# Kernel optimization log

Hardware: AMD Instinct MI355X
Metric: run time of the kernel (lower is better)

## Reference

```python
import jax, jax.numpy as jnp
import numpy as np

N = 100000
E = 1600000
D_IN = 64
D_HID = 64


def setup_inputs() -> dict:
    key = jax.random.key(0)
    k_x, k_e, k_w1, k_w2 = jax.random.split(key, 4)
    x = jax.random.normal(k_x, (N, D_IN), dtype=jnp.float32)
    edge_index = jax.random.randint(k_e, (2, E), 0, N, dtype=jnp.int64)
    # Glorot-ish init for GCNConv linear weights, bias zeros (PyG default bias=True)
    W1 = jax.random.normal(k_w1, (D_IN, D_HID), dtype=jnp.float32) * (1.0 / np.sqrt(D_IN))
    b1 = jnp.zeros((D_HID,), dtype=jnp.float32)
    W2 = jax.random.normal(k_w2, (D_HID, D_HID), dtype=jnp.float32) * (1.0 / np.sqrt(D_HID))
    b2 = jnp.zeros((D_HID,), dtype=jnp.float32)
    return {"x": x, "W1": W1, "b1": b1, "W2": W2, "b2": b2, "edge_index": edge_index}


def _gcn_norm(edge_index, n):
    # PyG GCNConv default: add self-loops, symmetric normalization D^-1/2 A D^-1/2
    loop = jnp.arange(n, dtype=edge_index.dtype)
    src = jnp.concatenate([edge_index[0], loop])  # [E+N] message sources (j)
    dst = jnp.concatenate([edge_index[1], loop])  # [E+N] message targets (i)
    ones = jnp.ones_like(dst, dtype=jnp.float32)
    deg = jax.ops.segment_sum(ones, dst, num_segments=n)  # in-degree incl. self-loop
    deg_inv_sqrt = jnp.where(deg > 0, jax.lax.rsqrt(deg), 0.0)
    norm = deg_inv_sqrt[src] * deg_inv_sqrt[dst]  # [E+N]
    return src, dst, norm


def _gcn_conv(x, W, b, src, dst, norm, n):
    h = x @ W                                   # [N, D_out] dense transform first
    msg = h[src] * norm[:, None]                # gather + edge scale, [E+N, D_out]
    out = jax.ops.segment_sum(msg, dst, num_segments=n)  # scatter-add to targets
    return out + b


def reference(x, W1, b1, W2, b2, edge_index):
    n = x.shape[0]
    src, dst, norm = _gcn_norm(edge_index, n)
    h = _gcn_conv(x, W1, b1, src, dst, norm, n)
    h = jax.nn.relu(h)
    out = _gcn_conv(h, W2, b2, src, dst, norm, n)
    return out
```

## Files before the change

### kernel.cpp

```cpp
#include <hip/hip_runtime.h>
#include <hip/hip_bf16.h>

constexpr int D = 64;
constexpr int CAP = 64;
constexpr int NBUCK = 8;

__global__ void k_fill_pad(const int* __restrict__ src, const int* __restrict__ dst,
                           int* __restrict__ cur, int* __restrict__ csr,
                           int e, int bdiv) {
    int p = blockIdx.x & (NBUCK - 1);
    int sub = blockIdx.x >> 3;
    int nsub = gridDim.x >> 3;
    int lo = p * bdiv, hi = lo + bdiv;
    for (int i = sub * blockDim.x + threadIdx.x; i < e; i += nsub * blockDim.x) {
        int d = dst[i];
        if (d >= lo && d < hi) {
            int r = atomicAdd(&cur[d], 1);
            if (r < CAP) csr[((size_t)d << 6) + r] = src[i];
        }
    }
}

__global__ void k_prep(const float* __restrict__ x, __hip_bfloat16* __restrict__ xb,
                       const int* __restrict__ cur, float* __restrict__ dinv, int n) {
    int stride = gridDim.x * blockDim.x;
    int i0 = blockIdx.x * blockDim.x + threadIdx.x;
    for (int i = i0; i < n; i += stride)
        dinv[i] = rsqrtf((float)cur[i] + 1.0f);
    int total = n * D;
    for (int i = i0; i < total; i += stride)
        xb[i] = __float2bfloat16(x[i]);
}

template <bool STORE_RELU_BF16>
__launch_bounds__(256, 2)
__global__ void k_agg_mm(const __hip_bfloat16* __restrict__ xin, const float* __restrict__ W,
                         const float* __restrict__ b, const int* __restrict__ csr,
                         const int* __restrict__ cnt, const float* __restrict__ dinv,
                         float* __restrict__ outf, __hip_bfloat16* __restrict__ outb, int n) {
    int lane = threadIdx.x & 63;
    float w[D];
#pragma unroll
    for (int k = 0; k < D; ++k) w[k] = W[k * D + lane];
    float bias = b[lane];

    int wv = __builtin_amdgcn_readfirstlane(threadIdx.x >> 6);
    int wave = blockIdx.x * (blockDim.x >> 6) + wv;
    int nwaves = gridDim.x * (blockDim.x >> 6);

    for (int node = wave; node < n; node += nwaves) {
        float dnode = dinv[node];
        float acc = __bfloat162float(xin[((size_t)node << 6) + lane]) * dnode;
        const int* __restrict__ row = csr + ((size_t)node << 6);
        int deg = cnt[node];
        deg = deg > CAP ? CAP : deg;
        int j = 0;
        for (; j + 7 < deg; j += 8) {
            int s0 = row[j], s1 = row[j + 1], s2 = row[j + 2], s3 = row[j + 3];
            int s4 = row[j + 4], s5 = row[j + 5], s6 = row[j + 6], s7 = row[j + 7];
            float v0 = __bfloat162float(xin[((size_t)s0 << 6) + lane]);
            float v1 = __bfloat162float(xin[((size_t)s1 << 6) + lane]);
            float v2 = __bfloat162float(xin[((size_t)s2 << 6) + lane]);
            float v3 = __bfloat162float(xin[((size_t)s3 << 6) + lane]);
            float v4 = __bfloat162float(xin[((size_t)s4 << 6) + lane]);
            float v5 = __bfloat162float(xin[((size_t)s5 << 6) + lane]);
            float v6 = __bfloat162float(xin[((size_t)s6 << 6) + lane]);
            float v7 = __bfloat162float(xin[((size_t)s7 << 6) + lane]);
            acc = fmaf(v0, dinv[s0], acc);
            acc = fmaf(v1, dinv[s1], acc);
            acc = fmaf(v2, dinv[s2], acc);
            acc = fmaf(v3, dinv[s3], acc);
            acc = fmaf(v4, dinv[s4], acc);
            acc = fmaf(v5, dinv[s5], acc);
            acc = fmaf(v6, dinv[s6], acc);
            acc = fmaf(v7, dinv[s7], acc);
        }
        for (; j < deg; ++j) {
            int s = row[j];
            acc = fmaf(__bfloat162float(xin[((size_t)s << 6) + lane]), dinv[s], acc);
        }
        acc *= dnode;

        int ab = __float_as_int(acc);
        float o0 = bias, o1 = 0.f;
#pragma unroll
        for (int k = 0; k < D; k += 2) {
            float a0 = __int_as_float(__builtin_amdgcn_readlane(ab, k));
            float a1 = __int_as_float(__builtin_amdgcn_readlane(ab, k + 1));
            o0 = fmaf(a0, w[k], o0);
            o1 = fmaf(a1, w[k + 1], o1);
        }
        float o = o0 + o1;
        if (STORE_RELU_BF16)
            outb[((size_t)node << 6) + lane] = __float2bfloat16(fmaxf(o, 0.f));
        else
            outf[((size_t)node << 6) + lane] = o;
    }
}

extern "C" void kernel_launch(void* const* d_in, const int* in_sizes, int n_in,
                              void* d_out, int out_size, void* d_ws, size_t ws_size,
                              hipStream_t stream) {
    const float* x  = (const float*)d_in[0];
    const float* W1 = (const float*)d_in[1];
    const float* b1 = (const float*)d_in[2];
    const float* W2 = (const float*)d_in[3];
    const float* b2 = (const float*)d_in[4];
    const int*   ei = (const int*)d_in[5];

    const int n = in_sizes[0] / D;
    const int e = in_sizes[5] / 2;
    const int* src = ei;
    const int* dst = ei + e;
    float* out = (float*)d_out;
    const int bdiv = (n + NBUCK - 1) / NBUCK;

    char* base = (char*)d_ws;
    auto alloc = [&](size_t bytes) {
        void* p = (void*)base;
        base += (bytes + 255) & ~(size_t)255;
        return p;
    };
    int*   cur  = (int*)alloc((size_t)n * 4);
    float* dinv = (float*)alloc((size_t)n * 4);
    int*   csr  = (int*)alloc((size_t)n * CAP * 4);
    __hip_bfloat16* xb  = (__hip_bfloat16*)alloc((size_t)n * D * 2);
    __hip_bfloat16* h1b = (__hip_bfloat16*)alloc((size_t)n * D * 2);

    const int B = 256;

    hipMemsetAsync(cur, 0, (size_t)n * 4, stream);
    k_fill_pad<<<2048, B, 0, stream>>>(src, dst, cur, csr, e, bdiv);
    k_prep<<<1024, B, 0, stream>>>(x, xb, cur, dinv, n);

    k_agg_mm<true><<<1024, B, 0, stream>>>(xb, W1, b1, csr, cur, dinv, nullptr, h1b, n);
    k_agg_mm<false><<<1024, B, 0, stream>>>(h1b, W2, b2, csr, cur, dinv, out, nullptr, n);
}
```

Before: 262.0 us.

## Pre-scale features by dinv, pad CSR rows with zero node, batch four nodes per wave

Source features are pre-multiplied by the source node's inverse-sqrt degree, in k_prep for layer 1 and in the layer-1 epilogue for h1, so the gather loop no longer loads dinv per edge. CSR rows are padded to multiples of 8 with a sentinel index that points at an extra zero row, which removes the scalar tail loop. Each wave now handles a contiguous chunk of nodes four at a time, which interleaves gathers from four rows for more memory parallelism. Weights are read inside the matvec loop instead of being held in 64 registers, and launch bounds rise to 4 blocks per CU for occupancy, at the cost of extra W loads and some wasted work on padded edges.

```diff
diff --git a/kernel.cpp b/kernel.cpp
--- a/kernel.cpp
+++ b/kernel.cpp
@@ -4,6 +4,8 @@
 constexpr int D = 64;
 constexpr int CAP = 64;
 constexpr int NBUCK = 8;
+
+#define BF2F(v) __bfloat162float(v)
 
 __global__ void k_fill_pad(const int* __restrict__ src, const int* __restrict__ dst,
                            int* __restrict__ cur, int* __restrict__ csr,
@@ -21,80 +23,123 @@
     }
 }
 
-__global__ void k_prep(const float* __restrict__ x, __hip_bfloat16* __restrict__ xb,
-                       const int* __restrict__ cur, float* __restrict__ dinv, int n) {
+__global__ void k_prep(const float* __restrict__ x, __hip_bfloat16* __restrict__ xs,
+                       __hip_bfloat16* __restrict__ h1s, const int* __restrict__ cur,
+                       float* __restrict__ dinv, int* __restrict__ csr, int n) {
     int stride = gridDim.x * blockDim.x;
     int i0 = blockIdx.x * blockDim.x + threadIdx.x;
-    for (int i = i0; i < n; i += stride)
-        dinv[i] = rsqrtf((float)cur[i] + 1.0f);
+    for (int i = i0; i < n; i += stride) {
+        int c = cur[i];
+        dinv[i] = rsqrtf((float)c + 1.0f);
+        int deg = c > CAP ? CAP : c;
+        int rd = (deg + 7) & ~7;
+        if (rd > CAP) rd = CAP;
+        for (int r = deg; r < rd; ++r) csr[((size_t)i << 6) + r] = n;
+    }
     int total = n * D;
-    for (int i = i0; i < total; i += stride)
-        xb[i] = __float2bfloat16(x[i]);
+    for (int idx = i0; idx < total; idx += stride) {
+        int i = idx >> 6;
+        float sc = rsqrtf((float)cur[i] + 1.0f);
+        xs[idx] = __float2bfloat16(x[idx] * sc);
+    }
+    if (i0 < D) {
+        xs[((size_t)n << 6) + i0] = __float2bfloat16(0.f);
+        h1s[((size_t)n << 6) + i0] = __float2bfloat16(0.f);
+    }
 }
 
-template <bool STORE_RELU_BF16>
-__launch_bounds__(256, 2)
-__global__ void k_agg_mm(const __hip_bfloat16* __restrict__ xin, const float* __restrict__ W,
-                         const float* __restrict__ b, const int* __restrict__ csr,
-                         const int* __restrict__ cnt, const float* __restrict__ dinv,
-                         float* __restrict__ outf, __hip_bfloat16* __restrict__ outb, int n) {
+template <bool L1>
+__launch_bounds__(256, 4)
+__global__ void k_agg_mm(const __hip_bfloat16* __restrict__ xs,
+                         const float* __restrict__ W, const float* __restrict__ b,
+                         const int* __restrict__ csr, const int* __restrict__ cnt,
+                         const float* __restrict__ dinv,
+                         float* __restrict__ outf, __hip_bfloat16* __restrict__ outb,
+                         int n, int chunk) {
     int lane = threadIdx.x & 63;
-    float w[D];
+    float bias = b[lane];
+    int wv = __builtin_amdgcn_readfirstlane(threadIdx.x >> 6);
+    int wave = blockIdx.x * 4 + wv;
+
+    int lo = wave * chunk;
+    int hi = lo + chunk;
+    if (hi > n) hi = n;
+
+    for (int nd = lo; nd < hi; nd += 4) {
+        int nn0 = nd, nn1 = nd + 1, nn2 = nd + 2, nn3 = nd + 3;
+        bool a1 = nn1 < hi, a2 = nn2 < hi, a3 = nn3 < hi;
+
+        int rd0 = 0, rd1 = 0, rd2 = 0, rd3 = 0;
+#define RDEG(k) { int c_ = cnt[nn##k]; int dg_ = c_ > CAP ? CAP : c_; \
+                  rd##k = (dg_ + 7) & ~7; if (rd##k > CAP) rd##k = CAP; }
+        RDEG(0) if (a1) RDEG(1) if (a2) RDEG(2) if (a3) RDEG(3)
+#undef RDEG
+        const int* __restrict__ r0 = csr + ((size_t)nn0 << 6);
+        const int* __restrict__ r1 = csr + ((size_t)nn1 << 6);
+        const int* __restrict__ r2 = csr + ((size_t)nn2 << 6);
+        const int* __restrict__ r3 = csr + ((size_t)nn3 << 6);
+
+        float acc0 = BF2F(xs[((size_t)nn0 << 6) + lane]);
+        float acc1 = a1 ? BF2F(xs[((size_t)nn1 << 6) + lane]) : 0.f;
+        float acc2 = a2 ? BF2F(xs[((size_t)nn2 << 6) + lane]) : 0.f;
+        float acc3 = a3 ? BF2F(xs[((size_t)nn3 << 6) + lane]) : 0.f;
+
+        int jm = rd0;
+        if (rd1 > jm) jm = rd1;
+        if (rd2 > jm) jm = rd2;
+        if (rd3 > jm) jm = rd3;
+
+        for (int j = 0; j < jm; j += 8) {
+#define GB(k)                                                                   \
+            if (j < rd##k) {                                                    \
+                int s0 = r##k[j],     s1 = r##k[j + 1],                         \
+                    s2 = r##k[j + 2], s3 = r##k[j + 3],                         \
+                    s4 = r##k[j + 4], s5 = r##k[j + 5],                         \
+                    s6 = r##k[j + 6], s7 = r##k[j + 7];                         \
+                float v0 = BF2F(xs[((size_t)s0 << 6) + lane]);                  \
+                float v1 = BF2F(xs[((size_t)s1 << 6) + lane]);                  \
+                float v2 = BF2F(xs[((size_t)s2 << 6) + lane]);                  \
+                float v3 = BF2F(xs[((size_t)s3 << 6) + lane]);                  \
+                float v4 = BF2F(xs[((size_t)s4 << 6) + lane]);                  \
+                float v5 = BF2F(xs[((size_t)s5 << 6) + lane]);                  \
+                float v6 = BF2F(xs[((size_t)s6 << 6) + lane]);                  \
+                float v7 = BF2F(xs[((size_t)s7 << 6) + lane]);                  \
+                acc##k += (((v0 + v1) + (v2 + v3)) + ((v4 + v5) + (v6 + v7)));  \
+            }
+            GB(0) GB(1) GB(2) GB(3)
+#undef GB
+        }
+
+        int ab0 = __float_as_int(acc0), ab1 = __float_as_int(acc1);
+        int ab2 = __float_as_int(acc2), ab3 = __float_as_int(acc3);
+        float p00 = 0.f, p01 = 0.f, p10 = 0.f, p11 = 0.f;
+        float p20 = 0.f, p21 = 0.f, p30 = 0.f, p31 = 0.f;
 #pragma unroll
-    for (int k = 0; k < D; ++k) w[k] = W[k * D + lane];
-    float bias = b[lane];
-
-    int wv = __builtin_amdgcn_readfirstlane(threadIdx.x >> 6);
-    int wave = blockIdx.x * (blockDim.x >> 6) + wv;
-    int nwaves = gridDim.x * (blockDim.x >> 6);
-
-    for (int node = wave; node < n; node += nwaves) {
-        float dnode = dinv[node];
-        float acc = __bfloat162float(xin[((size_t)node << 6) + lane]) * dnode;
-        const int* __restrict__ row = csr + ((size_t)node << 6);
-        int deg = cnt[node];
-        deg = deg > CAP ? CAP : deg;
-        int j = 0;
-        for (; j + 7 < deg; j += 8) {
-            int s0 = row[j], s1 = row[j + 1], s2 = row[j + 2], s3 = row[j + 3];
-            int s4 = row[j + 4], s5 = row[j + 5], s6 = row[j + 6], s7 = row[j + 7];
-            float v0 = __bfloat162float(xin[((size_t)s0 << 6) + lane]);
-            float v1 = __bfloat162float(xin[((size_t)s1 << 6) + lane]);
-            float v2 = __bfloat162float(xin[((size_t)s2 << 6) + lane]);
-            float v3 = __bfloat162float(xin[((size_t)s3 << 6) + lane]);
-            float v4 = __bfloat162float(xin[((size_t)s4 << 6) + lane]);
-            float v5 = __bfloat162float(xin[((size_t)s5 << 6) + lane]);
-            float v6 = __bfloat162float(xin[((size_t)s6 << 6) + lane]);
-            float v7 = __bfloat162float(xin[((size_t)s7 << 6) + lane]);
-            acc = fmaf(v0, dinv[s0], acc);
-            acc = fmaf(v1, dinv[s1], acc);
-            acc = fmaf(v2, dinv[s2], acc);
-            acc = fmaf(v3, dinv[s3], acc);
-            acc = fmaf(v4, dinv[s4], acc);
-            acc = fmaf(v5, dinv[s5], acc);
-            acc = fmaf(v6, dinv[s6], acc);
-            acc = fmaf(v7, dinv[s7], acc);
+        for (int kk = 0; kk < D; kk += 2) {
+            float w0 = W[kk * D + lane];
+            float w1 = W[(kk + 1) * D + lane];
+            p00 = fmaf(__int_as_float(__builtin_amdgcn_readlane(ab0, kk)),     w0, p00);
+            p01 = fmaf(__int_as_float(__builtin_amdgcn_readlane(ab0, kk + 1)), w1, p01);
+            p10 = fmaf(__int_as_float(__builtin_amdgcn_readlane(ab1, kk)),     w0, p10);
+            p11 = fmaf(__int_as_float(__builtin_amdgcn_readlane(ab1, kk + 1)), w1, p11);
+            p20 = fmaf(__int_as_float(__builtin_amdgcn_readlane(ab2, kk)),     w0, p20);
+            p21 = fmaf(__int_as_float(__builtin_amdgcn_readlane(ab2, kk + 1)), w1, p21);
+            p30 = fmaf(__int_as_float(__builtin_amdgcn_readlane(ab3, kk)),     w0, p30);
+            p31 = fmaf(__int_as_float(__builtin_amdgcn_readlane(ab3, kk + 1)), w1, p31);
         }
-        for (; j < deg; ++j) {
-            int s = row[j];
-            acc = fmaf(__bfloat162float(xin[((size_t)s << 6) + lane]), dinv[s], acc);
+#define EPI(k, pA, pB)                                                          \
+        {                                                                       \
+            float dn_ = dinv[nn##k];                                            \
+            float o_ = fmaf(dn_, pA + pB, bias);                                \
+            if (L1) outb[((size_t)nn##k << 6) + lane] =                         \
+                        __float2bfloat16(dn_ * fmaxf(o_, 0.f));                 \
+            else    outf[((size_t)nn##k << 6) + lane] = o_;                     \
         }
-        acc *= dnode;
-
-        int ab = __float_as_int(acc);
-        float o0 = bias, o1 = 0.f;
-#pragma unroll
-        for (int k = 0; k < D; k += 2) {
-            float a0 = __int_as_float(__builtin_amdgcn_readlane(ab, k));
-            float a1 = __int_as_float(__builtin_amdgcn_readlane(ab, k + 1));
-            o0 = fmaf(a0, w[k], o0);
-            o1 = fmaf(a1, w[k + 1], o1);
-        }
-        float o = o0 + o1;
-        if (STORE_RELU_BF16)
-            outb[((size_t)node << 6) + lane] = __float2bfloat16(fmaxf(o, 0.f));
-        else
-            outf[((size_t)node << 6) + lane] = o;
+        EPI(0, p00, p01)
+        if (a1) EPI(1, p10, p11)
+        if (a2) EPI(2, p20, p21)
+        if (a3) EPI(3, p30, p31)
+#undef EPI
     }
 }
 
@@ -123,16 +168,22 @@
     };
     int*   cur  = (int*)alloc((size_t)n * 4);
     float* dinv = (float*)alloc((size_t)n * 4);
-    int*   csr  = (int*)alloc((size_t)n * CAP * 4);
-    __hip_bfloat16* xb  = (__hip_bfloat16*)alloc((size_t)n * D * 2);
-    __hip_bfloat16* h1b = (__hip_bfloat16*)alloc((size_t)n * D * 2);
+    int*   csr  = (int*)alloc((size_t)(n + 1) * CAP * 4);
+    __hip_bfloat16* xs  = (__hip_bfloat16*)alloc((size_t)(n + 1) * D * 2);
+    __hip_bfloat16* h1s = (__hip_bfloat16*)alloc((size_t)(n + 1) * D * 2);
 
     const int B = 256;
+    const int AGG_BLOCKS = 2084;
+    const int nwaves = AGG_BLOCKS * 4;
+    int chunk = (n + nwaves - 1) / nwaves;
+    chunk = (chunk + 3) & ~3;
 
     hipMemsetAsync(cur, 0, (size_t)n * 4, stream);
     k_fill_pad<<<2048, B, 0, stream>>>(src, dst, cur, csr, e, bdiv);
-    k_prep<<<1024, B, 0, stream>>>(x, xb, cur, dinv, n);
+    k_prep<<<1024, B, 0, stream>>>(x, xs, h1s, cur, dinv, csr, n);
 
-    k_agg_mm<true><<<1024, B, 0, stream>>>(xb, W1, b1, csr, cur, dinv, nullptr, h1b, n);
-    k_agg_mm<false><<<1024, B, 0, stream>>>(h1b, W2, b2, csr, cur, dinv, out, nullptr, n);
+    k_agg_mm<true><<<AGG_BLOCKS, B, 0, stream>>>(xs, W1, b1, csr, cur, dinv,
+                                                 nullptr, h1s, n, chunk);
+    k_agg_mm<false><<<AGG_BLOCKS, B, 0, stream>>>(h1s, W2, b2, csr, cur, dinv,
+                                                  out, nullptr, n, chunk);
 }
```

Measured after the change: 441.4 us. +68.5%, slower.
